# Optimization experiments

Hardware: AMD Instinct MI355X
Metric: run time of the kernel (lower is better)

The kernel has to match this reference:

```python
import jax, jax.numpy as jnp
import numpy as np

DIM = 768
HEADS = 12
HEAD_DIM = DIM // HEADS
SCALE = HEAD_DIM ** -0.5
BATCH = 4      # B videos
FRAMES = 64    # f frames
NTOK = 128     # W_TP tokens per window


def setup_inputs() -> dict:
    key = jax.random.key(0)
    ks = jax.random.split(key, 6)
    x = jax.random.normal(ks[0], (BATCH * FRAMES, NTOK, DIM), jnp.float32)
    # binary mask per frame (zeros are later masked_fill'd to -10000)
    mask = (jax.random.uniform(ks[1], (FRAMES, NTOK, NTOK)) > 0.2).astype(jnp.float32)
    edge_bias = jax.random.normal(ks[2], (NTOK, NTOK), jnp.float32)
    qkv_w = jax.random.normal(ks[3], (3 * DIM, DIM), jnp.float32) * (DIM ** -0.5)
    qkv_b = jnp.zeros((3 * DIM,), jnp.float32)
    proj_w = jax.random.normal(ks[4], (DIM, DIM), jnp.float32) * (DIM ** -0.5)
    proj_b = jnp.zeros((DIM,), jnp.float32)
    return {"x": x, "mask": mask, "edge_bias": edge_bias,
            "qkv_w": qkv_w, "qkv_b": qkv_b,
            "proj_w": proj_w, "proj_b": proj_b,
            "B": BATCH, "f": FRAMES}


def reference(x, mask, edge_bias, qkv_w, qkv_b, proj_w, proj_b, B, f):
    B_f, N, D = x.shape
    H, Dh = HEADS, D // HEADS
    # qkv projection -> [3, B_f, H, N, Dh]
    qkv = (x @ qkv_w.T + qkv_b).reshape(B_f, N, 3, H, Dh)
    qkv = jnp.transpose(qkv, (2, 0, 3, 1, 4))
    q = qkv[0] * jnp.float32(SCALE)
    k = qkv[1]
    v = qkv[2]
    # raw scores [B_f, H, N, N]
    attn = jnp.einsum('bhnd,bhmd->bhnm', q, k)
    # mask multiply ([1,f,1,N,N]) and edge-bias multiply ([1,1,1,N,N])
    attn = attn.reshape(B, f, H, N, N)
    attn = attn * mask[None, :, None] * edge_bias[None, None, None]
    attn = attn.reshape(B_f, H, N, N)
    # masked_fill(attn == 0, -10000) then softmax of NEGATED scores
    attn = jnp.where(attn == 0.0, jnp.float32(-10000.0), attn)
    attn = jax.nn.softmax(-attn, axis=-1)
    out = jnp.einsum('bhnm,bhmd->bhnd', attn, v)  # [B_f,H,N,Dh]
    out = jnp.transpose(out, (0, 2, 1, 3)).reshape(B_f, N, D)
    return out @ proj_w.T + proj_b
```

## Files before the change

kernel.cpp:

```cpp
#include <hip/hip_runtime.h>

typedef unsigned short u16;
typedef unsigned int   u32;
typedef unsigned long long u64;

typedef __attribute__((ext_vector_type(8))) short bf16x8;
typedef __attribute__((ext_vector_type(4))) float f32x4;

__device__ __forceinline__ u16 rne_bf16(float f) {
  u32 u = __builtin_bit_cast(u32, f);
  u = (u + 0x7fffu + ((u >> 16) & 1u)) >> 16;
  return (u16)u;
}
__device__ __forceinline__ u32 pack_bf16x2(float lo, float hi) {
  return (u32)rne_bf16(lo) | ((u32)rne_bf16(hi) << 16);
}

__global__ __launch_bounds__(256)
void prep_masks(const float* __restrict__ mask,
                u64* __restrict__ bm0, u64* __restrict__ bm1,
                float* __restrict__ invc) {
  int row  = blockIdx.x * 4 + (threadIdx.x >> 6);
  int lane = threadIdx.x & 63;
  float v0 = mask[(long)row * 128 + lane];
  float v1 = mask[(long)row * 128 + 64 + lane];
  u64 b0 = __ballot(v0 == 0.0f);
  u64 b1 = __ballot(v1 == 0.0f);
  if (lane == 0) {
    bm0[row] = b0; bm1[row] = b1;
    int c = __builtin_popcountll(b0) + __builtin_popcountll(b1);
    invc[row] = c ? (1.0f / (float)c) : 0.0f;
  }
}

__global__ __launch_bounds__(256)
void transpose_wv(const float* __restrict__ qkv_w, u16* __restrict__ WvT) {
  __shared__ float tile[64][65];
  int tj = blockIdx.x % 12, td = blockIdx.x / 12;
  int t = threadIdx.x;
  const float* src = qkv_w + (long)1536 * 768 + (long)(tj * 64) * 768 + td * 64;
  #pragma unroll
  for (int i = 0; i < 4; ++i) {
    int j = (t >> 4) + 16 * i;
    int d = (t & 15) * 4;
    float4 v = *(const float4*)&src[(long)j * 768 + d];
    tile[j][d] = v.x; tile[j][d + 1] = v.y; tile[j][d + 2] = v.z; tile[j][d + 3] = v.w;
  }
  __syncthreads();
  u16* dst = WvT + (long)(td * 64) * 768 + tj * 64;
  #pragma unroll
  for (int i = 0; i < 4; ++i) {
    int d = (t >> 4) + 16 * i;
    int j = (t & 15) * 4;
    uint2 p;
    p.x = pack_bf16x2(tile[j][d],     tile[j + 1][d]);
    p.y = pack_bf16x2(tile[j + 2][d], tile[j + 3][d]);
    *(uint2*)&dst[(long)d * 768 + j] = p;
  }
}

__global__ __launch_bounds__(256)
void bias_combine(const float* __restrict__ proj_w, const float* __restrict__ qkv_b,
                  const float* __restrict__ proj_b, float* __restrict__ cbias) {
  int i = blockIdx.x * 4 + (threadIdx.x >> 6);
  int lane = threadIdx.x & 63;
  float s = 0.f;
  for (int j = lane; j < 768; j += 64) s += proj_w[(long)i * 768 + j] * qkv_b[1536 + j];
  #pragma unroll
  for (int off = 32; off; off >>= 1) s += __shfl_down(s, off);
  if (lane == 0) cbias[i] = s + proj_b[i];
}

template<bool A_FP32, bool BF16_OUT>
__global__ __launch_bounds__(256, 2)
void gemm_bt(const void* __restrict__ Av, const u16* __restrict__ Bm,
             void* __restrict__ Cv, const float* __restrict__ bias,
             int M, int N, int K, int nblk) {
  __shared__ u16 lA[2][128 * 32];
  __shared__ u16 lB[2][128 * 32];

  const int nwg = gridDim.x;
  const int bid = blockIdx.x;
  const int qq = nwg >> 3, rr8 = nwg & 7;
  const int xcd = bid & 7, loc = bid >> 3;
  const int swz = (xcd < rr8) ? (xcd * (qq + 1) + loc)
                              : (rr8 * (qq + 1) + (xcd - rr8) * qq + loc);
  const int mb = swz / nblk, nb = swz % nblk;
  const long arow0 = (long)mb * 128;
  const long brow0 = (long)nb * 128;

  const int tid = threadIdx.x;
  const int lane = tid & 63, wid = tid >> 6;
  const int wr = wid >> 1, wc = wid & 1;

  const u16* Ab  = (const u16*)Av;
  const float* Af = (const float*)Av;

  const int nk = K >> 5;

  f32x4 acc[4][4];
  const f32x4 vzero = {0.f, 0.f, 0.f, 0.f};
  #pragma unroll
  for (int i = 0; i < 4; ++i)
    #pragma unroll
    for (int j = 0; j < 4; ++j) acc[i][j] = vzero;

  auto stage = [&](int buf, int kt) {
    #pragma unroll
    for (int i = 0; i < 2; ++i) {
      int tt = tid + 256 * i;
      const u16* g = &Bm[(brow0 + (tt >> 2)) * (long)K + kt * 32 + 8 * (tt & 3)];
      __builtin_amdgcn_global_load_lds(
          static_cast<const u32*>(static_cast<const void*>(g)),
          static_cast<u32*>(static_cast<void*>(&lB[buf][512 * wid + 2048 * i])),
          16, 0, 0);
    }
    if constexpr (A_FP32) {
      #pragma unroll
      for (int i = 0; i < 4; ++i) {
        int row = 32 * i + (tid >> 3);
        int kk = 4 * (tid & 7);
        float4 v = *(const float4*)&Af[(arow0 + row) * (long)K + kt * 32 + kk];
        uint2 p;
        p.x = pack_bf16x2(v.x, v.y);
        p.y = pack_bf16x2(v.z, v.w);
        *(uint2*)&lA[buf][row * 32 + kk] = p;
      }
    } else {
      #pragma unroll
      for (int i = 0; i < 2; ++i) {
        int tt = tid + 256 * i;
        const u16* g = &Ab[(arow0 + (tt >> 2)) * (long)K + kt * 32 + 8 * (tt & 3)];
        __builtin_amdgcn_global_load_lds(
            static_cast<const u32*>(static_cast<const void*>(g)),
            static_cast<u32*>(static_cast<void*>(&lA[buf][512 * wid + 2048 * i])),
            16, 0, 0);
      }
    }
  };

  stage(0, 0);
  __syncthreads();

  int cur = 0;
  for (int kt = 0; kt < nk; ++kt) {
    if (kt + 1 < nk) stage(cur ^ 1, kt + 1);
    bf16x8 afr[4], bfr[4];
    #pragma unroll
    for (int i = 0; i < 4; ++i) {
      afr[i] = *(const bf16x8*)&lA[cur][(64 * wr + 16 * i + (lane & 15)) * 32 + 8 * (lane >> 4)];
      bfr[i] = *(const bf16x8*)&lB[cur][(64 * wc + 16 * i + (lane & 15)) * 32 + 8 * (lane >> 4)];
    }
    #pragma unroll
    for (int mi = 0; mi < 4; ++mi)
      #pragma unroll
      for (int ni = 0; ni < 4; ++ni)
        acc[mi][ni] = __builtin_amdgcn_mfma_f32_16x16x32_bf16(afr[mi], bfr[ni], acc[mi][ni], 0, 0, 0);
    __syncthreads();
    cur ^= 1;
  }

  const long orow = arow0 + 64 * wr;
  const long ocol = brow0 + 64 * wc;
  #pragma unroll
  for (int mi = 0; mi < 4; ++mi) {
    #pragma unroll
    for (int ni = 0; ni < 4; ++ni) {
      #pragma unroll
      for (int e = 0; e < 4; ++e) {
        long row = orow + 16 * mi + 4 * (lane >> 4) + e;
        long col = ocol + 16 * ni + (lane & 15);
        float v = acc[mi][ni][e];
        if constexpr (BF16_OUT) {
          ((u16*)Cv)[row * N + col] = rne_bf16(v);
        } else {
          ((float*)Cv)[row * N + col] = v + bias[col];
        }
      }
    }
  }
}

__global__ __launch_bounds__(256, 2)
void avg_mfma(const float* __restrict__ x,
              const u64* __restrict__ bm0, const u64* __restrict__ bm1,
              const float* __restrict__ invc, u16* __restrict__ Z) {
  __shared__ u16 lM[128 * 128];
  __shared__ u16 lx[128 * 128];

  const int bid = blockIdx.x;
  const int bfi = bid / 6;
  const int ch  = bid - bfi * 6;
  const int fr  = bfi & 63;
  const int tid = threadIdx.x;
  const int lane = tid & 63, wid = tid >> 6;
  const int wr = wid >> 1, wc = wid & 1;

  {
    int n = tid >> 1, h = tid & 1;
    u64 bits = h ? bm1[fr * 128 + n] : bm0[fr * 128 + n];
    char* orow = (char*)&lM[n * 128];
    #pragma unroll
    for (int g = 0; g < 8; ++g) {
      u64 w0 = 0, w1 = 0;
      #pragma unroll
      for (int j = 0; j < 4; ++j) {
        if ((bits >> (8 * g + j)) & 1)     w0 |= (u64)0x3f80u << (16 * j);
        if ((bits >> (8 * g + 4 + j)) & 1) w1 |= (u64)0x3f80u << (16 * j);
      }
      int gran = (8 * h + g) ^ (n & 15);
      *(u64*)(orow + gran * 16)     = w0;
      *(u64*)(orow + gran * 16 + 8) = w1;
    }
  }

  {
    const float* xs = x + (long)bfi * 128 * 768 + ch * 128;
    const int dl = tid & 31;
    const int mq = tid >> 5;
    #pragma unroll 4
    for (int cc = 0; cc < 16; ++cc) {
      int d  = dl + 32 * (cc & 3);
      int m0 = 4 * (mq + 8 * (cc >> 2));
      float v0 = xs[(long)(m0 + 0) * 768 + d];
      float v1 = xs[(long)(m0 + 1) * 768 + d];
      float v2 = xs[(long)(m0 + 2) * 768 + d];
      float v3 = xs[(long)(m0 + 3) * 768 + d];
      uint2 p;
      p.x = pack_bf16x2(v0, v1);
      p.y = pack_bf16x2(v2, v3);
      int byte = d * 256 + ((m0 * 2) ^ ((d & 15) << 4));
      *(uint2*)((char*)lx + byte) = p;
    }
  }
  __syncthreads();

  f32x4 acc[4][4];
  const f32x4 vzero = {0.f, 0.f, 0.f, 0.f};
  #pragma unroll
  for (int i = 0; i < 4; ++i)
    #pragma unroll
    for (int j = 0; j < 4; ++j) acc[i][j] = vzero;

  #pragma unroll
  for (int kk = 0; kk < 4; ++kk) {
    const int kb = 64 * kk + 16 * (lane >> 4);
    bf16x8 afr[4], bfr[4];
    #pragma unroll
    for (int i = 0; i < 4; ++i) {
      int n = 64 * wr + 16 * i + (lane & 15);
      afr[i] = *(const bf16x8*)((char*)lM + n * 256 + (kb ^ ((n & 15) << 4)));
      int d = 64 * wc + 16 * i + (lane & 15);
      bfr[i] = *(const bf16x8*)((char*)lx + d * 256 + (kb ^ ((d & 15) << 4)));
    }
    #pragma unroll
    for (int mi = 0; mi < 4; ++mi)
      #pragma unroll
      for (int ni = 0; ni < 4; ++ni)
        acc[mi][ni] = __builtin_amdgcn_mfma_f32_16x16x32_bf16(afr[mi], bfr[ni], acc[mi][ni], 0, 0, 0);
  }

  const float* icp = invc + fr * 128;
  u16* zp = Z + ((long)bfi * 128) * 768 + ch * 128;
  #pragma unroll
  for (int mi = 0; mi < 4; ++mi) {
    #pragma unroll
    for (int e = 0; e < 4; ++e) {
      int n = 64 * wr + 16 * mi + 4 * (lane >> 4) + e;
      float ic = icp[n];
      #pragma unroll
      for (int ni = 0; ni < 4; ++ni) {
        int d = 64 * wc + 16 * ni + (lane & 15);
        zp[(long)n * 768 + d] = rne_bf16(acc[mi][ni][e] * ic);
      }
    }
  }
}

extern "C" void kernel_launch(void* const* d_in, const int* in_sizes, int n_in,
                              void* d_out, int out_size, void* d_ws, size_t ws_size,
                              hipStream_t stream) {
  (void)in_sizes; (void)n_in; (void)out_size; (void)ws_size;
  const float* x      = (const float*)d_in[0];
  const float* mask   = (const float*)d_in[1];
  const float* qkv_w  = (const float*)d_in[3];
  const float* qkv_b  = (const float*)d_in[4];
  const float* proj_w = (const float*)d_in[5];
  const float* proj_b = (const float*)d_in[6];

  char* w = (char*)d_ws;
  u16*   WvT  = (u16*)(w);
  u16*   Wc   = (u16*)(w + 0x120000);
  float* cb   = (float*)(w + 0x240000);
  u64*   bm0  = (u64*)(w + 0x241000);
  u64*   bm1  = (u64*)(w + 0x251000);
  float* invc = (float*)(w + 0x261000);
  u16*   Z    = (u16*)(w + 0x270000);

  prep_masks<<<dim3(2048), dim3(256), 0, stream>>>(mask, bm0, bm1, invc);
  transpose_wv<<<dim3(144), dim3(256), 0, stream>>>(qkv_w, WvT);
  bias_combine<<<dim3(192), dim3(256), 0, stream>>>(proj_w, qkv_b, proj_b, cb);
  gemm_bt<true, true><<<dim3(36), dim3(256), 0, stream>>>(
      (const void*)proj_w, WvT, (void*)Wc, nullptr, 768, 768, 768, 6);
  avg_mfma<<<dim3(1536), dim3(256), 0, stream>>>(x, bm0, bm1, invc, Z);
  gemm_bt<false, false><<<dim3(1536), dim3(256), 0, stream>>>(
      (const void*)Z, Wc, d_out, cb, 32768, 768, 768, 6);
}
```

Before: 126.9 us.

## Swizzle LDS tiles, swap MFMA operands for vectorized stores, widen x loads

Adds XOR swizzles to the GEMM LDS tiles, applied both on the global_load_lds source offsets and on the fragment reads, to cut bank conflicts. It also swaps the MFMA operand order so each lane holds four consecutive output columns, which allows float4/uint2 stores in the GEMM and averaging epilogues. The averaging kernel loads x with float4, uses an extended swizzle, and the GEMM launch bounds rise to four waves per SIMD. The risks are register pressure under the tighter launch bound and correctness of the matched swizzle mappings; the B_FP32 template path is added but not used.

```diff
diff --git a/kernel.cpp b/kernel.cpp
--- a/kernel.cpp
+++ b/kernel.cpp
@@ -71,9 +71,9 @@
   if (lane == 0) cbias[i] = s + proj_b[i];
 }
 
-template<bool A_FP32, bool BF16_OUT>
-__global__ __launch_bounds__(256, 2)
-void gemm_bt(const void* __restrict__ Av, const u16* __restrict__ Bm,
+template<bool A_FP32, bool B_FP32, bool BF16_OUT>
+__global__ __launch_bounds__(256, 4)
+void gemm_bt(const void* __restrict__ Av, const void* __restrict__ Bv,
              void* __restrict__ Cv, const float* __restrict__ bias,
              int M, int N, int K, int nblk) {
   __shared__ u16 lA[2][128 * 32];
@@ -93,9 +93,6 @@
   const int lane = tid & 63, wid = tid >> 6;
   const int wr = wid >> 1, wc = wid & 1;
 
-  const u16* Ab  = (const u16*)Av;
-  const float* Af = (const float*)Av;
-
   const int nk = K >> 5;
 
   f32x4 acc[4][4];
@@ -106,31 +103,48 @@
     for (int j = 0; j < 4; ++j) acc[i][j] = vzero;
 
   auto stage = [&](int buf, int kt) {
-    #pragma unroll
-    for (int i = 0; i < 2; ++i) {
-      int tt = tid + 256 * i;
-      const u16* g = &Bm[(brow0 + (tt >> 2)) * (long)K + kt * 32 + 8 * (tt & 3)];
-      __builtin_amdgcn_global_load_lds(
-          static_cast<const u32*>(static_cast<const void*>(g)),
-          static_cast<u32*>(static_cast<void*>(&lB[buf][512 * wid + 2048 * i])),
-          16, 0, 0);
+    if constexpr (B_FP32) {
+      const float* Bf = (const float*)Bv;
+      #pragma unroll
+      for (int i = 0; i < 4; ++i) {
+        int row = 32 * i + (tid >> 3);
+        int kk = 4 * (tid & 7);
+        float4 v = *(const float4*)&Bf[(brow0 + row) * (long)K + kt * 32 + kk];
+        uint2 p; p.x = pack_bf16x2(v.x, v.y); p.y = pack_bf16x2(v.z, v.w);
+        int byte = row * 64 + ((8 * (tid & 7)) ^ (((row >> 1) & 3) << 4));
+        *(uint2*)((char*)&lB[buf][0] + byte) = p;
+      }
+    } else {
+      const u16* Bb = (const u16*)Bv;
+      #pragma unroll
+      for (int i = 0; i < 2; ++i) {
+        int tt = tid + 256 * i;
+        int gsrc = (tt & 3) ^ ((tt >> 3) & 3);
+        const u16* g = &Bb[(brow0 + (tt >> 2)) * (long)K + kt * 32 + 8 * gsrc];
+        __builtin_amdgcn_global_load_lds(
+            static_cast<const u32*>(static_cast<const void*>(g)),
+            static_cast<u32*>(static_cast<void*>(&lB[buf][512 * wid + 2048 * i])),
+            16, 0, 0);
+      }
     }
     if constexpr (A_FP32) {
+      const float* Af = (const float*)Av;
       #pragma unroll
       for (int i = 0; i < 4; ++i) {
         int row = 32 * i + (tid >> 3);
         int kk = 4 * (tid & 7);
         float4 v = *(const float4*)&Af[(arow0 + row) * (long)K + kt * 32 + kk];
-        uint2 p;
-        p.x = pack_bf16x2(v.x, v.y);
-        p.y = pack_bf16x2(v.z, v.w);
-        *(uint2*)&lA[buf][row * 32 + kk] = p;
+        uint2 p; p.x = pack_bf16x2(v.x, v.y); p.y = pack_bf16x2(v.z, v.w);
+        int byte = row * 64 + ((8 * (tid & 7)) ^ (((row >> 1) & 3) << 4));
+        *(uint2*)((char*)&lA[buf][0] + byte) = p;
       }
     } else {
+      const u16* Ab = (const u16*)Av;
       #pragma unroll
       for (int i = 0; i < 2; ++i) {
         int tt = tid + 256 * i;
-        const u16* g = &Ab[(arow0 + (tt >> 2)) * (long)K + kt * 32 + 8 * (tt & 3)];
+        int gsrc = (tt & 3) ^ ((tt >> 3) & 3);
+        const u16* g = &Ab[(arow0 + (tt >> 2)) * (long)K + kt * 32 + 8 * gsrc];
         __builtin_amdgcn_global_load_lds(
             static_cast<const u32*>(static_cast<const void*>(g)),
             static_cast<u32*>(static_cast<void*>(&lA[buf][512 * wid + 2048 * i])),
@@ -148,34 +162,39 @@
     bf16x8 afr[4], bfr[4];
     #pragma unroll
     for (int i = 0; i < 4; ++i) {
-      afr[i] = *(const bf16x8*)&lA[cur][(64 * wr + 16 * i + (lane & 15)) * 32 + 8 * (lane >> 4)];
-      bfr[i] = *(const bf16x8*)&lB[cur][(64 * wc + 16 * i + (lane & 15)) * 32 + 8 * (lane >> 4)];
-    }
-    #pragma unroll
-    for (int mi = 0; mi < 4; ++mi)
-      #pragma unroll
-      for (int ni = 0; ni < 4; ++ni)
-        acc[mi][ni] = __builtin_amdgcn_mfma_f32_16x16x32_bf16(afr[mi], bfr[ni], acc[mi][ni], 0, 0, 0);
+      int ra = 64 * wr + 16 * i + (lane & 15);
+      afr[i] = *(const bf16x8*)((const char*)&lA[cur][0] +
+                ra * 64 + ((16 * (lane >> 4)) ^ (((ra >> 1) & 3) << 4)));
+      int rb = 64 * wc + 16 * i + (lane & 15);
+      bfr[i] = *(const bf16x8*)((const char*)&lB[cur][0] +
+                rb * 64 + ((16 * (lane >> 4)) ^ (((rb >> 1) & 3) << 4)));
+    }
+    #pragma unroll
+    for (int b = 0; b < 4; ++b)
+      #pragma unroll
+      for (int a = 0; a < 4; ++a)
+        acc[b][a] = __builtin_amdgcn_mfma_f32_16x16x32_bf16(bfr[b], afr[a], acc[b][a], 0, 0, 0);
     __syncthreads();
     cur ^= 1;
   }
 
-  const long orow = arow0 + 64 * wr;
-  const long ocol = brow0 + 64 * wc;
-  #pragma unroll
-  for (int mi = 0; mi < 4; ++mi) {
-    #pragma unroll
-    for (int ni = 0; ni < 4; ++ni) {
-      #pragma unroll
-      for (int e = 0; e < 4; ++e) {
-        long row = orow + 16 * mi + 4 * (lane >> 4) + e;
-        long col = ocol + 16 * ni + (lane & 15);
-        float v = acc[mi][ni][e];
-        if constexpr (BF16_OUT) {
-          ((u16*)Cv)[row * N + col] = rne_bf16(v);
-        } else {
-          ((float*)Cv)[row * N + col] = v + bias[col];
-        }
+  #pragma unroll
+  for (int b = 0; b < 4; ++b) {
+    long n0 = brow0 + 64 * wc + 16 * b + 4 * (lane >> 4);
+    #pragma unroll
+    for (int a = 0; a < 4; ++a) {
+      long m = arow0 + 64 * wr + 16 * a + (lane & 15);
+      if constexpr (BF16_OUT) {
+        uint2 p;
+        p.x = pack_bf16x2(acc[b][a][0], acc[b][a][1]);
+        p.y = pack_bf16x2(acc[b][a][2], acc[b][a][3]);
+        *(uint2*)&((u16*)Cv)[m * N + n0] = p;
+      } else {
+        const float4 bb = *(const float4*)&bias[n0];
+        float4 o;
+        o.x = acc[b][a][0] + bb.x; o.y = acc[b][a][1] + bb.y;
+        o.z = acc[b][a][2] + bb.z; o.w = acc[b][a][3] + bb.w;
+        *(float4*)&((float*)Cv)[m * N + n0] = o;
       }
     }
   }
@@ -198,6 +217,7 @@
 
   {
     int n = tid >> 1, h = tid & 1;
+    int sw = (n & 15) ^ ((n >> 4) & 3);
     u64 bits = h ? bm1[fr * 128 + n] : bm0[fr * 128 + n];
     char* orow = (char*)&lM[n * 128];
     #pragma unroll
@@ -208,7 +228,7 @@
         if ((bits >> (8 * g + j)) & 1)     w0 |= (u64)0x3f80u << (16 * j);
         if ((bits >> (8 * g + 4 + j)) & 1) w1 |= (u64)0x3f80u << (16 * j);
       }
-      int gran = (8 * h + g) ^ (n & 15);
+      int gran = (8 * h + g) ^ sw;
       *(u64*)(orow + gran * 16)     = w0;
       *(u64*)(orow + gran * 16 + 8) = w1;
     }
@@ -216,21 +236,25 @@
 
   {
     const float* xs = x + (long)bfi * 128 * 768 + ch * 128;
-    const int dl = tid & 31;
-    const int mq = tid >> 5;
-    #pragma unroll 4
-    for (int cc = 0; cc < 16; ++cc) {
-      int d  = dl + 32 * (cc & 3);
-      int m0 = 4 * (mq + 8 * (cc >> 2));
-      float v0 = xs[(long)(m0 + 0) * 768 + d];
-      float v1 = xs[(long)(m0 + 1) * 768 + d];
-      float v2 = xs[(long)(m0 + 2) * 768 + d];
-      float v3 = xs[(long)(m0 + 3) * 768 + d];
-      uint2 p;
-      p.x = pack_bf16x2(v0, v1);
-      p.y = pack_bf16x2(v2, v3);
-      int byte = d * 256 + ((m0 * 2) ^ ((d & 15) << 4));
-      *(uint2*)((char*)lx + byte) = p;
+    const int d4  = 4 * (tid & 31);
+    const int mq8 = tid >> 5;
+    #pragma unroll
+    for (int cc = 0; cc < 4; ++cc) {
+      int q  = mq8 + 8 * cc;
+      int m0 = 4 * q;
+      float4 v0 = *(const float4*)&xs[(long)(m0 + 0) * 768 + d4];
+      float4 v1 = *(const float4*)&xs[(long)(m0 + 1) * 768 + d4];
+      float4 v2 = *(const float4*)&xs[(long)(m0 + 2) * 768 + d4];
+      float4 v3 = *(const float4*)&xs[(long)(m0 + 3) * 768 + d4];
+      #pragma unroll
+      for (int dd = 0; dd < 4; ++dd) {
+        int d = d4 + dd;
+        int sw = ((d & 15) ^ ((d >> 4) & 3)) << 4;
+        uint2 p;
+        p.x = pack_bf16x2((&v0.x)[dd], (&v1.x)[dd]);
+        p.y = pack_bf16x2((&v2.x)[dd], (&v3.x)[dd]);
+        *(uint2*)((char*)lx + d * 256 + ((8 * q) ^ sw)) = p;
+      }
     }
   }
   __syncthreads();
@@ -244,14 +268,16 @@
 
   #pragma unroll
   for (int kk = 0; kk < 4; ++kk) {
-    const int kb = 64 * kk + 16 * (lane >> 4);
+    const int klog = 64 * kk + 16 * (lane >> 4);
     bf16x8 afr[4], bfr[4];
     #pragma unroll
     for (int i = 0; i < 4; ++i) {
-      int n = 64 * wr + 16 * i + (lane & 15);
-      afr[i] = *(const bf16x8*)((char*)lM + n * 256 + (kb ^ ((n & 15) << 4)));
-      int d = 64 * wc + 16 * i + (lane & 15);
-      bfr[i] = *(const bf16x8*)((char*)lx + d * 256 + (kb ^ ((d & 15) << 4)));
+      int d = 64 * wr + 16 * i + (lane & 15);
+      int swd = ((d & 15) ^ ((d >> 4) & 3)) << 4;
+      afr[i] = *(const bf16x8*)((char*)lx + d * 256 + (klog ^ swd));
+      int n = 64 * wc + 16 * i + (lane & 15);
+      int swn = ((n & 15) ^ ((n >> 4) & 3)) << 4;
+      bfr[i] = *(const bf16x8*)((char*)lM + n * 256 + (klog ^ swn));
     }
     #pragma unroll
     for (int mi = 0; mi < 4; ++mi)
@@ -261,18 +287,18 @@
   }
 
   const float* icp = invc + fr * 128;
-  u16* zp = Z + ((long)bfi * 128) * 768 + ch * 128;
-  #pragma unroll
-  for (int mi = 0; mi < 4; ++mi) {
-    #pragma unroll
-    for (int e = 0; e < 4; ++e) {
-      int n = 64 * wr + 16 * mi + 4 * (lane >> 4) + e;
-      float ic = icp[n];
-      #pragma unroll
-      for (int ni = 0; ni < 4; ++ni) {
-        int d = 64 * wc + 16 * ni + (lane & 15);
-        zp[(long)n * 768 + d] = rne_bf16(acc[mi][ni][e] * ic);
-      }
+  u16* zp = Z + (long)bfi * 128 * 768 + ch * 128;
+  #pragma unroll
+  for (int ni = 0; ni < 4; ++ni) {
+    int n = 64 * wc + 16 * ni + (lane & 15);
+    float ic = icp[n];
+    #pragma unroll
+    for (int mi = 0; mi < 4; ++mi) {
+      int d0 = 64 * wr + 16 * mi + 4 * (lane >> 4);
+      uint2 p;
+      p.x = pack_bf16x2(acc[mi][ni][0] * ic, acc[mi][ni][1] * ic);
+      p.y = pack_bf16x2(acc[mi][ni][2] * ic, acc[mi][ni][3] * ic);
+      *(uint2*)&zp[(long)n * 768 + d0] = p;
     }
   }
 }
@@ -300,9 +326,9 @@
   prep_masks<<<dim3(2048), dim3(256), 0, stream>>>(mask, bm0, bm1, invc);
   transpose_wv<<<dim3(144), dim3(256), 0, stream>>>(qkv_w, WvT);
   bias_combine<<<dim3(192), dim3(256), 0, stream>>>(proj_w, qkv_b, proj_b, cb);
-  gemm_bt<true, true><<<dim3(36), dim3(256), 0, stream>>>(
-      (const void*)proj_w, WvT, (void*)Wc, nullptr, 768, 768, 768, 6);
+  gemm_bt<true, false, true><<<dim3(36), dim3(256), 0, stream>>>(
+      (const void*)proj_w, (const void*)WvT, (void*)Wc, nullptr, 768, 768, 768, 6);
   avg_mfma<<<dim3(1536), dim3(256), 0, stream>>>(x, bm0, bm1, invc, Z);
-  gemm_bt<false, false><<<dim3(1536), dim3(256), 0, stream>>>(
-      (const void*)Z, Wc, d_out, cb, 32768, 768, 768, 6);
-}
+  gemm_bt<false, false, false><<<dim3(1536), dim3(256), 0, stream>>>(
+      (const void*)Z, (const void*)Wc, d_out, cb, 32768, 768, 768, 6);
+}
```

Result: slower. 132.8 us (+4.7%).
